# Kernel tuning notes

Hardware: AMD Instinct MI355X
Metric: run time of the kernel (lower is better)

## Reference

```python
import jax, jax.numpy as jnp
import numpy as np

TAU = 2.0        # LIF membrane time constant
VTH = 1.0        # firing threshold
ALPHA = 4.0      # surrogate sigmoid sharpness
BN_EPS = 1e-5

@jax.custom_vjp
def heaviside_surrogate(x):
    # Forward: hard threshold. Backward: sigmoid surrogate gradient (alpha=4).
    return (x >= 0.0).astype(x.dtype)

def _hs_fwd(x):
    return heaviside_surrogate(x), x

def _hs_bwd(x, g):
    s = jax.nn.sigmoid(ALPHA * x)
    return (g * ALPHA * s * (1.0 - s),)

heaviside_surrogate.defvjp(_hs_fwd, _hs_bwd)


def setup_inputs() -> dict:
    key = jax.random.key(0)
    k1, k2 = jax.random.split(key)
    B, Cin, T, Cout = 64, 512, 1024, 256
    x = jax.random.normal(k1, (B, Cin, T), dtype=jnp.float32)
    W = jax.random.normal(k2, (Cout, Cin), dtype=jnp.float32) * (1.0 / np.sqrt(Cin))
    gamma = jnp.ones((Cout,), dtype=jnp.float32)
    beta = jnp.zeros((Cout,), dtype=jnp.float32)
    run_mean = jnp.zeros((Cout,), dtype=jnp.float32)
    run_var = jnp.ones((Cout,), dtype=jnp.float32)
    return {"x": x, "W": W, "gamma": gamma, "beta": beta,
            "run_mean": run_mean, "run_var": run_var}


def reference(x, W, gamma, beta, run_mean, run_var):
    # Dropout is identity in eval mode.
    # conv1d, kernel_size=1, no bias -> pointwise GEMM over channels: [B,Cin,T] -> [B,Cout,T]
    y = jnp.einsum('bct,oc->bot', x, W)
    # BatchNorm1d (inference, running stats), per-channel affine
    inv = jax.lax.rsqrt(run_var + BN_EPS)
    y = (y - run_mean[None, :, None]) * (inv * gamma)[None, :, None] + beta[None, :, None]
    # LIF recurrence over the time dim (last axis), hard reset to 0, detach_reset.
    yt = jnp.transpose(y, (2, 0, 1))  # [T, B, Cout]

    def step(v, x_t):
        v = v + (x_t - v) / TAU              # decay_input charge
        s = heaviside_surrogate(v - VTH)     # spike via surrogate threshold
        v = v * (1.0 - jax.lax.stop_gradient(s))  # hard reset (detached)
        return v, s

    v0 = jnp.zeros(yt.shape[1:], dtype=yt.dtype)
    _, spikes = jax.lax.scan(step, v0, yt)   # spikes: [T, B, Cout]
    # out.mean(dim=-1) == spike rate over time
    return spikes.mean(axis=0)               # [B, Cout]
```

## Files before the change

### kernel.cpp

```cpp
#include <hip/hip_runtime.h>
#include <math.h>

typedef __attribute__((ext_vector_type(8)))  __bf16 bf16v8;
typedef __attribute__((ext_vector_type(16))) float  f32x16;
typedef __attribute__((ext_vector_type(4)))  float  f32x4;

namespace {
constexpr int kB = 64, kCin = 512, kT = 1024, kCout = 256;
constexpr size_t kYBytes    = (size_t)kB * kT * kCout * 4;
constexpr size_t kWfragBytes = (size_t)32 * 8 * 3 * 64 * 16;
constexpr size_t kSBytes    = kCout * 4;
constexpr size_t kWsNeed    = kYBytes + kWfragBytes + kSBytes;
}

__global__ void wsplit_kernel(const float* __restrict__ W, __bf16* __restrict__ wfrag) {
    const int kc = blockIdx.x, osub = blockIdx.y, p = blockIdx.z;
    const int lane = threadIdx.x;
    const int o  = osub * 32 + (lane & 31);
    const int kb = kc * 16 + (lane >> 5) * 8;
    bf16v8 frag;
#pragma unroll
    for (int j = 0; j < 8; ++j) {
        const float w = W[o * kCin + kb + j];
        const __bf16 h = (__bf16)w;
        const float r1 = w - (float)h;
        const __bf16 m = (__bf16)r1;
        const float r2 = r1 - (float)m;
        const __bf16 l = (__bf16)r2;
        frag[j] = (p == 0) ? h : (p == 1) ? m : l;
    }
    const size_t idx = ((size_t)(kc * 8 + osub) * 3 + p) * 64 + lane;
    *reinterpret_cast<bf16v8*>(wfrag + idx * 8) = frag;
}

__global__ void sprep_kernel(const float* __restrict__ gamma, const float* __restrict__ rvar,
                             float* __restrict__ sarr) {
    const int o = threadIdx.x;
    sarr[o] = (float)((double)gamma[o] / sqrt((double)rvar[o] + 1e-5));
}

__global__ __launch_bounds__(512, 2)
void gemm_split_kernel(const float* __restrict__ x, const __bf16* __restrict__ wfrag,
                       const float* __restrict__ sarr, const float* __restrict__ rmean,
                       const float* __restrict__ beta, float* __restrict__ y) {
    __shared__ float tbuf[8 * 32 * 36];
    const int tid  = threadIdx.x;
    const int lane = tid & 63;
    const int wave = tid >> 6;
    const int wo = wave >> 1, wt = wave & 1;
    const int n = lane & 31, q = lane >> 5;
    const int b  = blockIdx.y;
    const int o0 = wo * 64;
    const int t0 = blockIdx.x * 128 + wt * 64;
    const float* __restrict__ xb = x + ((size_t)b << 19);
    const bf16v8* __restrict__ wf = reinterpret_cast<const bf16v8*>(wfrag);

    f32x16 acc[2][2] = {};

    float  xr[2][2][8];
    bf16v8 ar[2][2][3];

    auto loadk = [&](int kc, float (&xd)[2][8], bf16v8 (&ad)[2][3]) {
#pragma unroll
        for (int s = 0; s < 2; ++s)
#pragma unroll
            for (int j = 0; j < 8; ++j)
                xd[s][j] = xb[(size_t)(kc * 16 + q * 8 + j) * kT + t0 + s * 32 + n];
#pragma unroll
        for (int i = 0; i < 2; ++i)
#pragma unroll
            for (int p = 0; p < 3; ++p)
                ad[i][p] = wf[(size_t)((kc * 8 + wo * 2 + i) * 3 + p) * 64 + lane];
    };

    auto compute = [&](const float (&xd)[2][8], const bf16v8 (&ad)[2][3]) {
        bf16v8 Bh[2], Bm[2], Bl[2];
#pragma unroll
        for (int s = 0; s < 2; ++s) {
#pragma unroll
            for (int j = 0; j < 8; ++j) {
                const float f = xd[s][j];
                const __bf16 h = (__bf16)f;
                const float r1 = f - (float)h;
                const __bf16 m = (__bf16)r1;
                const float r2 = r1 - (float)m;
                const __bf16 l = (__bf16)r2;
                Bh[s][j] = h; Bm[s][j] = m; Bl[s][j] = l;
            }
        }
#pragma unroll
        for (int i = 0; i < 2; ++i)
#pragma unroll
            for (int s = 0; s < 2; ++s) {
                f32x16 a = acc[i][s];
                a = __builtin_amdgcn_mfma_f32_32x32x16_bf16(ad[i][0], Bh[s], a, 0, 0, 0);
                a = __builtin_amdgcn_mfma_f32_32x32x16_bf16(ad[i][0], Bm[s], a, 0, 0, 0);
                a = __builtin_amdgcn_mfma_f32_32x32x16_bf16(ad[i][1], Bh[s], a, 0, 0, 0);
                a = __builtin_amdgcn_mfma_f32_32x32x16_bf16(ad[i][0], Bl[s], a, 0, 0, 0);
                a = __builtin_amdgcn_mfma_f32_32x32x16_bf16(ad[i][2], Bh[s], a, 0, 0, 0);
                a = __builtin_amdgcn_mfma_f32_32x32x16_bf16(ad[i][1], Bm[s], a, 0, 0, 0);
                acc[i][s] = a;
            }
    };

    loadk(0, xr[0], ar[0]);
    for (int kc2 = 0; kc2 < 16; ++kc2) {
        loadk(2 * kc2 + 1, xr[1], ar[1]);
        compute(xr[0], ar[0]);
        if (kc2 < 15) loadk(2 * kc2 + 2, xr[0], ar[0]);
        compute(xr[1], ar[1]);
    }

    float* tb = tbuf + wave * (32 * 36);
#pragma unroll
    for (int i = 0; i < 2; ++i)
#pragma unroll
        for (int s = 0; s < 2; ++s) {
            asm volatile("s_waitcnt lgkmcnt(0)" ::: "memory");
#pragma unroll
            for (int g = 0; g < 4; ++g) {
                f32x4 v;
                v.x = acc[i][s][4 * g + 0];
                v.y = acc[i][s][4 * g + 1];
                v.z = acc[i][s][4 * g + 2];
                v.w = acc[i][s][4 * g + 3];
                *reinterpret_cast<f32x4*>(tb + n * 36 + g * 8 + q * 4) = v;
            }
            asm volatile("s_waitcnt lgkmcnt(0)" ::: "memory");
#pragma unroll
            for (int r4 = 0; r4 < 4; ++r4) {
                const int fidx = lane + 64 * r4;
                const int tl = fidx >> 3, o4 = fidx & 7;
                const int og = o0 + i * 32 + o4 * 4;
                f32x4 val = *reinterpret_cast<const f32x4*>(tb + tl * 36 + o4 * 4);
                const f32x4 sv = *reinterpret_cast<const f32x4*>(sarr + og);
                const f32x4 mv = *reinterpret_cast<const f32x4*>(rmean + og);
                const f32x4 bv = *reinterpret_cast<const f32x4*>(beta + og);
                val = (val - mv) * sv + bv;
                const size_t t = (size_t)t0 + s * 32 + tl;
                *reinterpret_cast<f32x4*>(y + ((((size_t)b << 10) + t) << 8) + og) = val;
            }
        }
}

__global__ __launch_bounds__(64)
void lif_kernel(const float* __restrict__ y, float* __restrict__ out) {
    const int b = blockIdx.x >> 2;
    const int o = ((blockIdx.x & 3) << 6) + threadIdx.x;
    const float* __restrict__ yb = y + ((size_t)b << 18);
    float v = 0.f;
    int cnt = 0;
    float b0[32], b1[32];
    auto loadb = [&](int i, float (&buf)[32]) {
#pragma unroll
        for (int j = 0; j < 32; ++j)
            buf[j] = yb[(size_t)(i * 32 + j) * 256 + o];
    };
    auto stepb = [&](const float (&buf)[32]) {
#pragma unroll
        for (int j = 0; j < 32; ++j) {
            v = v + (buf[j] - v) * 0.5f;
            if (v - 1.0f >= 0.0f) { ++cnt; v = 0.f; }
        }
    };
    loadb(0, b0);
    for (int bb = 0; bb < 16; ++bb) {
        loadb(2 * bb + 1, b1);
        stepb(b0);
        if (bb < 15) loadb(2 * bb + 2, b0);
        stepb(b1);
    }
    out[((size_t)b << 8) + o] = (float)cnt * (1.0f / 1024.0f);
}

namespace fb {
constexpr int kOTile = 32, kTTile = 128, kCc = 64;
constexpr int kNtt = kT / kTTile, kNcc = kCin / kCc, kYPad = 132;
}

__global__ void wt_transpose_kernel(const float* __restrict__ W, float* __restrict__ Wt) {
    int idx = blockIdx.x * 256 + threadIdx.x;
    int c = idx >> 8, o = idx & 255;
    Wt[idx] = W[o * kCin + c];
}

__global__ __launch_bounds__(256, 2)
void snn_fused_kernel(const float* __restrict__ x, const float* __restrict__ Wt,
                      const float* __restrict__ gamma, const float* __restrict__ beta,
                      const float* __restrict__ rmean, const float* __restrict__ rvar,
                      float* __restrict__ out) {
    using namespace fb;
    __shared__ float xs[kCc][kTTile];
    __shared__ float ws[kCc][kOTile];
    __shared__ float ytile[kOTile][kYPad];
    __shared__ float sarr[kOTile], barr[kOTile], marr[kOTile], vstate[kOTile];
    __shared__ int scnt[kOTile];
    const int tid = threadIdx.x, tx = tid & 31, ty = tid >> 5;
    const int b = blockIdx.y, o_blk = blockIdx.x * kOTile;
    if (tid < kOTile) {
        const int o = o_blk + tid;
        const double dinv = 1.0 / sqrt((double)rvar[o] + 1e-5);
        sarr[tid] = (float)(dinv * (double)gamma[o]);
        barr[tid] = beta[o]; marr[tid] = rmean[o];
        vstate[tid] = 0.0f; scnt[tid] = 0;
    }
    __syncthreads();
    const float* xb = x + (size_t)b * kCin * kT;
    for (int tt = 0; tt < kNtt; ++tt) {
        float acc[4][4];
#pragma unroll
        for (int i = 0; i < 4; ++i)
#pragma unroll
            for (int j = 0; j < 4; ++j) acc[i][j] = 0.0f;
        const int t0 = tt * kTTile;
        for (int cc = 0; cc < kNcc; ++cc) {
#pragma unroll
            for (int k = 0; k < 8; ++k) {
                const int f = tid + 256 * k;
                const int c = f >> 5, tq = f & 31;
                *reinterpret_cast<float4*>(&xs[c][tq * 4]) = *reinterpret_cast<const float4*>(
                    xb + (size_t)(cc * kCc + c) * kT + t0 + tq * 4);
            }
#pragma unroll
            for (int k = 0; k < 2; ++k) {
                const int f = tid + 256 * k;
                const int c = f >> 3, oq = f & 7;
                *reinterpret_cast<float4*>(&ws[c][oq * 4]) = *reinterpret_cast<const float4*>(
                    Wt + (size_t)(cc * kCc + c) * kCout + o_blk + oq * 4);
            }
            __syncthreads();
#pragma unroll 8
            for (int c = 0; c < kCc; ++c) {
                const float4 xv = *reinterpret_cast<const float4*>(&xs[c][tx * 4]);
                const float4 wv = *reinterpret_cast<const float4*>(&ws[c][ty * 4]);
                const float xf[4] = {xv.x, xv.y, xv.z, xv.w};
                const float wf4[4] = {wv.x, wv.y, wv.z, wv.w};
#pragma unroll
                for (int i = 0; i < 4; ++i)
#pragma unroll
                    for (int j = 0; j < 4; ++j) acc[i][j] += wf4[i] * xf[j];
            }
            __syncthreads();
        }
#pragma unroll
        for (int i = 0; i < 4; ++i) {
            const int o = ty * 4 + i;
            const float s = sarr[o], bb2 = barr[o], m = marr[o];
#pragma unroll
            for (int j = 0; j < 4; ++j) ytile[o][tx * 4 + j] = (acc[i][j] - m) * s + bb2;
        }
        __syncthreads();
        if (tid < kOTile) {
            float vv = vstate[tid];
            int cnt = 0;
#pragma unroll 4
            for (int t = 0; t < kTTile; ++t) {
                const float yv = ytile[tid][t];
                vv = vv + (yv - vv) * 0.5f;
                if (vv - 1.0f >= 0.0f) { cnt++; vv = 0.0f; }
            }
            vstate[tid] = vv; scnt[tid] += cnt;
        }
        __syncthreads();
    }
    if (tid < kOTile) out[b * kCout + o_blk + tid] = (float)scnt[tid] * (1.0f / 1024.0f);
}

extern "C" void kernel_launch(void* const* d_in, const int* in_sizes, int n_in,
                              void* d_out, int out_size, void* d_ws, size_t ws_size,
                              hipStream_t stream) {
    const float* x     = (const float*)d_in[0];
    const float* W     = (const float*)d_in[1];
    const float* gamma = (const float*)d_in[2];
    const float* beta  = (const float*)d_in[3];
    const float* rmean = (const float*)d_in[4];
    const float* rvar  = (const float*)d_in[5];
    float* out = (float*)d_out;

    if (ws_size >= kWsNeed) {
        float*  y     = (float*)d_ws;
        __bf16* wfrag = (__bf16*)((char*)d_ws + kYBytes);
        float*  sarr  = (float*)((char*)d_ws + kYBytes + kWfragBytes);
        sprep_kernel<<<1, 256, 0, stream>>>(gamma, rvar, sarr);
        wsplit_kernel<<<dim3(32, 8, 3), 64, 0, stream>>>(W, wfrag);
        gemm_split_kernel<<<dim3(8, 64), 512, 0, stream>>>(x, wfrag, sarr, rmean, beta, y);
        lif_kernel<<<256, 64, 0, stream>>>(y, out);
    } else {
        float* Wt = (float*)d_ws;
        wt_transpose_kernel<<<(kCin * kCout) / 256, 256, 0, stream>>>(W, Wt);
        snn_fused_kernel<<<dim3(kCout / fb::kOTile, kB), 256, 0, stream>>>(
            x, Wt, gamma, beta, rmean, rvar, out);
    }
}
```

Baseline: 283.8 us.

## Replace 3-way bf16 split GEMM with scaled 2-way fp16 split and LDS-staged X

The emulated-fp32 GEMM now splits W and x into scaled fp16 hi/lo pairs instead of bf16 hi/mid/lo triples. This cuts MFMAs per product from 6 to 3, with scaling chosen to keep residuals in fp16 range. x is now converted once per block and shared through double-buffered LDS with a swizzle, rather than each wave converting its own copy. The tile becomes 64 time steps per block over twice as many blocks. This risks fp16 range and precision problems that could flip spikes near threshold, and it adds a barrier every k-step.

```diff
diff --git a/kernel.cpp b/kernel.cpp
--- a/kernel.cpp
+++ b/kernel.cpp
@@ -1,36 +1,34 @@
 #include <hip/hip_runtime.h>
 #include <math.h>
 
-typedef __attribute__((ext_vector_type(8)))  __bf16 bf16v8;
-typedef __attribute__((ext_vector_type(16))) float  f32x16;
-typedef __attribute__((ext_vector_type(4)))  float  f32x4;
+typedef _Float16 f16;
+typedef __attribute__((ext_vector_type(8)))  _Float16 f16v8;
+typedef __attribute__((ext_vector_type(16))) float    f32x16;
+typedef __attribute__((ext_vector_type(4)))  float    f32x4;
 
 namespace {
 constexpr int kB = 64, kCin = 512, kT = 1024, kCout = 256;
-constexpr size_t kYBytes    = (size_t)kB * kT * kCout * 4;
-constexpr size_t kWfragBytes = (size_t)32 * 8 * 3 * 64 * 16;
-constexpr size_t kSBytes    = kCout * 4;
-constexpr size_t kWsNeed    = kYBytes + kWfragBytes + kSBytes;
-}
-
-__global__ void wsplit_kernel(const float* __restrict__ W, __bf16* __restrict__ wfrag) {
+constexpr size_t kYBytes     = (size_t)kB * kT * kCout * 4;
+constexpr size_t kWfragBytes = (size_t)32 * 8 * 2 * 64 * 16;
+constexpr size_t kSBytes     = kCout * 4;
+constexpr size_t kWsNeed     = kYBytes + kWfragBytes + kSBytes;
+}
+
+__global__ void wsplit16_kernel(const float* __restrict__ W, f16* __restrict__ wfrag) {
     const int kc = blockIdx.x, osub = blockIdx.y, p = blockIdx.z;
     const int lane = threadIdx.x;
     const int o  = osub * 32 + (lane & 31);
     const int kb = kc * 16 + (lane >> 5) * 8;
-    bf16v8 frag;
+    f16v8 frag;
 #pragma unroll
     for (int j = 0; j < 8; ++j) {
-        const float w = W[o * kCin + kb + j];
-        const __bf16 h = (__bf16)w;
-        const float r1 = w - (float)h;
-        const __bf16 m = (__bf16)r1;
-        const float r2 = r1 - (float)m;
-        const __bf16 l = (__bf16)r2;
-        frag[j] = (p == 0) ? h : (p == 1) ? m : l;
-    }
-    const size_t idx = ((size_t)(kc * 8 + osub) * 3 + p) * 64 + lane;
-    *reinterpret_cast<bf16v8*>(wfrag + idx * 8) = frag;
+        const float w = 32.0f * W[o * kCin + kb + j];
+        const f16 h = (f16)w;
+        const float r = w - (float)h;
+        const f16 l = (f16)(r * 2048.0f);
+        frag[j] = p ? l : h;
+    }
+    *reinterpret_cast<f16v8*>(wfrag + ((size_t)((kc * 8 + osub) * 2 + p) * 64 + lane) * 8) = frag;
 }
 
 __global__ void sprep_kernel(const float* __restrict__ gamma, const float* __restrict__ rvar,
@@ -40,107 +38,110 @@
 }
 
 __global__ __launch_bounds__(512, 2)
-void gemm_split_kernel(const float* __restrict__ x, const __bf16* __restrict__ wfrag,
-                       const float* __restrict__ sarr, const float* __restrict__ rmean,
-                       const float* __restrict__ beta, float* __restrict__ y) {
-    __shared__ float tbuf[8 * 32 * 36];
+void gemm_f16_kernel(const float* __restrict__ x, const f16* __restrict__ wfrag,
+                     const float* __restrict__ sarr, const float* __restrict__ rmean,
+                     const float* __restrict__ beta, float* __restrict__ y) {
+    __shared__ union {
+        f16   B[2][2][64 * 24];
+        float tb[8][32 * 36];
+    } sh;
+
     const int tid  = threadIdx.x;
     const int lane = tid & 63;
     const int wave = tid >> 6;
     const int wo = wave >> 1, wt = wave & 1;
     const int n = lane & 31, q = lane >> 5;
-    const int b  = blockIdx.y;
-    const int o0 = wo * 64;
-    const int t0 = blockIdx.x * 128 + wt * 64;
+    const int b   = blockIdx.y;
+    const int tg0 = blockIdx.x * 64;
+    const int o0  = wo * 64;
     const float* __restrict__ xb = x + ((size_t)b << 19);
-    const bf16v8* __restrict__ wf = reinterpret_cast<const bf16v8*>(wfrag);
-
-    f32x16 acc[2][2] = {};
-
-    float  xr[2][2][8];
-    bf16v8 ar[2][2][3];
-
-    auto loadk = [&](int kc, float (&xd)[2][8], bf16v8 (&ad)[2][3]) {
-#pragma unroll
-        for (int s = 0; s < 2; ++s)
-#pragma unroll
-            for (int j = 0; j < 8; ++j)
-                xd[s][j] = xb[(size_t)(kc * 16 + q * 8 + j) * kT + t0 + s * 32 + n];
+    const f16v8* __restrict__ wf = reinterpret_cast<const f16v8*>(wfrag);
+
+    const int st_t = lane;
+    const int st_k = wave;
+    const int wrow = st_t * 24 + 2 * (st_k ^ ((st_t >> 3 & 1) << 2));
+    const int tloc = wt * 32 + n;
+    const int rrow = tloc * 24 + 8 * (q ^ (tloc >> 3 & 1));
+
+    f32x16 accA[2] = {};
+    f32x16 accB[2] = {};
+    f16v8  af[2][2][2];
+    float  x0a, x1a;
+
+    auto loadX = [&](int kc) {
+        const float* px = xb + (size_t)(kc * 16 + 2 * st_k) * kT + tg0 + st_t;
+        x0a = px[0];
+        x1a = px[kT];
+    };
+    auto loadA = [&](int kc, f16v8 (&ad)[2][2]) {
 #pragma unroll
         for (int i = 0; i < 2; ++i)
 #pragma unroll
-            for (int p = 0; p < 3; ++p)
-                ad[i][p] = wf[(size_t)((kc * 8 + wo * 2 + i) * 3 + p) * 64 + lane];
-    };
-
-    auto compute = [&](const float (&xd)[2][8], const bf16v8 (&ad)[2][3]) {
-        bf16v8 Bh[2], Bm[2], Bl[2];
-#pragma unroll
-        for (int s = 0; s < 2; ++s) {
-#pragma unroll
-            for (int j = 0; j < 8; ++j) {
-                const float f = xd[s][j];
-                const __bf16 h = (__bf16)f;
-                const float r1 = f - (float)h;
-                const __bf16 m = (__bf16)r1;
-                const float r2 = r1 - (float)m;
-                const __bf16 l = (__bf16)r2;
-                Bh[s][j] = h; Bm[s][j] = m; Bl[s][j] = l;
-            }
-        }
-#pragma unroll
-        for (int i = 0; i < 2; ++i)
-#pragma unroll
-            for (int s = 0; s < 2; ++s) {
-                f32x16 a = acc[i][s];
-                a = __builtin_amdgcn_mfma_f32_32x32x16_bf16(ad[i][0], Bh[s], a, 0, 0, 0);
-                a = __builtin_amdgcn_mfma_f32_32x32x16_bf16(ad[i][0], Bm[s], a, 0, 0, 0);
-                a = __builtin_amdgcn_mfma_f32_32x32x16_bf16(ad[i][1], Bh[s], a, 0, 0, 0);
-                a = __builtin_amdgcn_mfma_f32_32x32x16_bf16(ad[i][0], Bl[s], a, 0, 0, 0);
-                a = __builtin_amdgcn_mfma_f32_32x32x16_bf16(ad[i][2], Bh[s], a, 0, 0, 0);
-                a = __builtin_amdgcn_mfma_f32_32x32x16_bf16(ad[i][1], Bm[s], a, 0, 0, 0);
-                acc[i][s] = a;
-            }
-    };
-
-    loadk(0, xr[0], ar[0]);
-    for (int kc2 = 0; kc2 < 16; ++kc2) {
-        loadk(2 * kc2 + 1, xr[1], ar[1]);
-        compute(xr[0], ar[0]);
-        if (kc2 < 15) loadk(2 * kc2 + 2, xr[0], ar[0]);
-        compute(xr[1], ar[1]);
-    }
-
-    float* tb = tbuf + wave * (32 * 36);
-#pragma unroll
-    for (int i = 0; i < 2; ++i)
-#pragma unroll
-        for (int s = 0; s < 2; ++s) {
-            asm volatile("s_waitcnt lgkmcnt(0)" ::: "memory");
-#pragma unroll
-            for (int g = 0; g < 4; ++g) {
-                f32x4 v;
-                v.x = acc[i][s][4 * g + 0];
-                v.y = acc[i][s][4 * g + 1];
-                v.z = acc[i][s][4 * g + 2];
-                v.w = acc[i][s][4 * g + 3];
-                *reinterpret_cast<f32x4*>(tb + n * 36 + g * 8 + q * 4) = v;
-            }
-            asm volatile("s_waitcnt lgkmcnt(0)" ::: "memory");
-#pragma unroll
-            for (int r4 = 0; r4 < 4; ++r4) {
-                const int fidx = lane + 64 * r4;
-                const int tl = fidx >> 3, o4 = fidx & 7;
-                const int og = o0 + i * 32 + o4 * 4;
-                f32x4 val = *reinterpret_cast<const f32x4*>(tb + tl * 36 + o4 * 4);
-                const f32x4 sv = *reinterpret_cast<const f32x4*>(sarr + og);
-                const f32x4 mv = *reinterpret_cast<const f32x4*>(rmean + og);
-                const f32x4 bv = *reinterpret_cast<const f32x4*>(beta + og);
-                val = (val - mv) * sv + bv;
-                const size_t t = (size_t)t0 + s * 32 + tl;
-                *reinterpret_cast<f32x4*>(y + ((((size_t)b << 10) + t) << 8) + og) = val;
-            }
-        }
+            for (int p = 0; p < 2; ++p)
+                ad[i][p] = wf[(size_t)((kc * 8 + wo * 2 + i) * 2 + p) * 64 + lane];
+    };
+    auto stage = [&](int buf) {
+        auto h2 = __builtin_amdgcn_cvt_pkrtz(x0a, x1a);
+        const float r0 = x0a - (float)h2[0];
+        const float r1 = x1a - (float)h2[1];
+        auto l2 = __builtin_amdgcn_cvt_pkrtz(r0 * 2048.0f, r1 * 2048.0f);
+        *reinterpret_cast<decltype(h2)*>(&sh.B[buf][0][wrow]) = h2;
+        *reinterpret_cast<decltype(l2)*>(&sh.B[buf][1][wrow]) = l2;
+    };
+    auto domfma = [&](int buf, const f16v8 (&ad)[2][2]) {
+        const f16v8 bh = *reinterpret_cast<const f16v8*>(&sh.B[buf][0][rrow]);
+        const f16v8 bl = *reinterpret_cast<const f16v8*>(&sh.B[buf][1][rrow]);
+#pragma unroll
+        for (int i = 0; i < 2; ++i) {
+            accA[i] = __builtin_amdgcn_mfma_f32_32x32x16_f16(ad[i][0], bh, accA[i], 0, 0, 0);
+            accB[i] = __builtin_amdgcn_mfma_f32_32x32x16_f16(ad[i][0], bl, accB[i], 0, 0, 0);
+            accB[i] = __builtin_amdgcn_mfma_f32_32x32x16_f16(ad[i][1], bh, accB[i], 0, 0, 0);
+        }
+    };
+
+    loadX(0);
+    loadA(0, af[0]);
+    stage(0);
+    loadX(1);
+    __syncthreads();
+
+#pragma unroll 2
+    for (int kc = 0; kc < 32; ++kc) {
+        const int cur = kc & 1, nxt = cur ^ 1;
+        if (kc < 31) loadA(kc + 1, af[nxt]);
+        if (kc < 31) stage(nxt);
+        if (kc < 30) loadX(kc + 2);
+        domfma(cur, af[cur]);
+        __syncthreads();
+    }
+
+    float* tb = sh.tb[wave];
+#pragma unroll
+    for (int i = 0; i < 2; ++i) {
+        const f32x16 v = accA[i] + accB[i] * 4.8828125e-4f;
+        asm volatile("s_waitcnt lgkmcnt(0)" ::: "memory");
+#pragma unroll
+        for (int g = 0; g < 4; ++g) {
+            f32x4 t4;
+            t4.x = v[4 * g + 0]; t4.y = v[4 * g + 1];
+            t4.z = v[4 * g + 2]; t4.w = v[4 * g + 3];
+            *reinterpret_cast<f32x4*>(tb + n * 36 + g * 8 + q * 4) = t4;
+        }
+        asm volatile("s_waitcnt lgkmcnt(0)" ::: "memory");
+#pragma unroll
+        for (int r4 = 0; r4 < 4; ++r4) {
+            const int fidx = lane + 64 * r4;
+            const int tl = fidx >> 3, o4 = fidx & 7;
+            const int og = o0 + i * 32 + o4 * 4;
+            f32x4 val = *reinterpret_cast<const f32x4*>(tb + tl * 36 + o4 * 4);
+            const f32x4 sv = *reinterpret_cast<const f32x4*>(sarr + og);
+            const f32x4 mv = *reinterpret_cast<const f32x4*>(rmean + og);
+            const f32x4 bv = *reinterpret_cast<const f32x4*>(beta + og);
+            val = (val * 0.03125f - mv) * sv + bv;
+            const size_t t = (size_t)tg0 + wt * 32 + tl;
+            *reinterpret_cast<f32x4*>(y + ((((size_t)b << 10) + t) << 8) + og) = val;
+        }
+    }
 }
 
 __global__ __launch_bounds__(64)
@@ -278,12 +279,12 @@
     float* out = (float*)d_out;
 
     if (ws_size >= kWsNeed) {
-        float*  y     = (float*)d_ws;
-        __bf16* wfrag = (__bf16*)((char*)d_ws + kYBytes);
-        float*  sarr  = (float*)((char*)d_ws + kYBytes + kWfragBytes);
+        float* y     = (float*)d_ws;
+        f16*   wfrag = (f16*)((char*)d_ws + kYBytes);
+        float* sarr  = (float*)((char*)d_ws + kYBytes + kWfragBytes);
         sprep_kernel<<<1, 256, 0, stream>>>(gamma, rvar, sarr);
-        wsplit_kernel<<<dim3(32, 8, 3), 64, 0, stream>>>(W, wfrag);
-        gemm_split_kernel<<<dim3(8, 64), 512, 0, stream>>>(x, wfrag, sarr, rmean, beta, y);
+        wsplit16_kernel<<<dim3(32, 8, 2), 64, 0, stream>>>(W, wfrag);
+        gemm_f16_kernel<<<dim3(16, 64), 512, 0, stream>>>(x, wfrag, sarr, rmean, beta, y);
         lif_kernel<<<256, 64, 0, stream>>>(y, out);
     } else {
         float* Wt = (float*)d_ws;
```

New measurement: 263.9 us. -7.0%, faster.
